# Kernel optimization log

Measured on AMD Instinct MI355X. Metric: run time of the kernel, lower is better.

The kernel has to match this reference:

```python
import jax, jax.numpy as jnp
import numpy as np

B, S, E, H = 4, 2048, 2048, 16
D = E // H  # head_dim = 128


def _rotary_tables():
    # standard interleaved RoPE: pairs (2i, 2i+1) share an angle
    inv_freq = 1.0 / (10000.0 ** (np.arange(0, D, 2, dtype=np.float64) / D))
    ang = np.arange(S, dtype=np.float64)[:, None] * inv_freq[None, :]  # [S, D/2]
    ang = np.repeat(ang, 2, axis=-1)  # [S, D]
    cos = np.cos(ang).astype(np.float32)[None, None]  # [1,1,S,D]
    sin = np.sin(ang).astype(np.float32)[None, None]
    return jnp.asarray(cos), jnp.asarray(sin)


def setup_inputs() -> dict:
    key = jax.random.key(0)
    ks = jax.random.split(key, 4)
    x = jax.random.normal(ks[0], (B, S, E), jnp.float32)
    cos, sin = _rotary_tables()
    Wqkv = jax.random.normal(ks[1], (E, 3 * E), jnp.float32) * 0.02
    bqkv = jnp.zeros((3 * E,), jnp.float32)
    Wproj = jax.random.normal(ks[2], (E, E), jnp.float32) * 0.02
    bproj = jnp.zeros((E,), jnp.float32)
    return {"x": x, "rotary_cos": cos, "rotary_sin": sin,
            "Wqkv": Wqkv, "bqkv": bqkv, "Wproj": Wproj, "bproj": bproj}


def apply_rotary(t, cos, sin):
    # t: [B,H,S,D]; interleaved rotate-half: (x1,x2) -> (-x2, x1)
    x1 = t[..., 0::2]
    x2 = t[..., 1::2]
    rot = jnp.stack((-x2, x1), axis=-1).reshape(t.shape)
    return t * cos + rot * sin


def reference(x, rotary_cos, rotary_sin, Wqkv, bqkv, Wproj, bproj):
    qkv = x @ Wqkv + bqkv  # [B,S,3E]
    q, k, v = jnp.split(qkv, 3, axis=-1)
    # [B,S,E] -> [B,H,S,D]
    to_heads = lambda t: t.reshape(B, S, H, D).transpose(0, 2, 1, 3)
    q, k, v = to_heads(q), to_heads(k), to_heads(v)
    q = apply_rotary(q, rotary_cos, rotary_sin)
    k = apply_rotary(k, rotary_cos, rotary_sin)
    scale = 1.0 / jnp.sqrt(jnp.float32(D))
    scores = jnp.einsum("bhqd,bhkd->bhqk", q, k) * scale  # non-causal
    attn = jax.nn.softmax(scores, axis=-1)
    y = jnp.einsum("bhqk,bhkd->bhqd", attn, v)
    y = y.transpose(0, 2, 1, 3).reshape(B, S, E)
    out = y @ Wproj + bproj
    return out, k, v
```

## Files before the change

### kernel.cpp

```cpp
#include <hip/hip_runtime.h>


typedef unsigned short u16;
typedef unsigned int   u32;
typedef float  f32x4  __attribute__((ext_vector_type(4)));
typedef __bf16 bf16x8 __attribute__((ext_vector_type(8)));

#define B_  4
#define S_  2048
#define E_  2048
#define H_  16
#define D_  128

__device__ __forceinline__ u16 f2bf(float f) {
    union { float f; u32 u; } v; v.f = f;
    return (u16)((v.u + 0x8000u) >> 16);
}
__device__ __forceinline__ u32 pack_bf(float a, float b) {
    union { float f; u32 u; } x, y; x.f = a; y.f = b;
    return ((x.u + 0x8000u) >> 16) | ((y.u + 0x8000u) & 0xFFFF0000u);
}
__device__ __forceinline__ float bf2f(u16 h) {
    union { u32 u; float f; } v; v.u = ((u32)h) << 16; return v.f;
}

__device__ __forceinline__ void gld16(const u16* g, u16* l) {
    __builtin_amdgcn_global_load_lds(
        (const __attribute__((address_space(1))) void*)g,
        (__attribute__((address_space(3))) void*)l, 16, 0, 0);
}

__global__ __launch_bounds__(256) void xconv_kernel(
    const float* __restrict__ x, u16* __restrict__ xb)
{
    size_t g = (size_t)blockIdx.x * 256 + threadIdx.x;
    const float4* p = (const float4*)x + g * 2;
    float4 a = p[0], b = p[1];
    uint4 pk;
    pk.x = pack_bf(a.x, a.y); pk.y = pack_bf(a.z, a.w);
    pk.z = pack_bf(b.x, b.y); pk.w = pack_bf(b.z, b.w);
    ((uint4*)xb)[g] = pk;
}

__global__ __launch_bounds__(256) void wtrans_kernel(
    const float* __restrict__ W, u16* __restrict__ WT, int K, int N)
{
    __shared__ float tile[64][65];
    const int n0 = blockIdx.x * 64, k0 = blockIdx.y * 64;
    const int t = threadIdx.x;
#pragma unroll
    for (int i = 0; i < 16; ++i) {
        int idx = i * 256 + t; int r = idx >> 6, c = idx & 63;
        tile[r][c] = W[(size_t)(k0 + r) * N + n0 + c];
    }
    __syncthreads();
#pragma unroll
    for (int i = 0; i < 16; ++i) {
        int idx = i * 256 + t; int rn = idx >> 6, ck = idx & 63;
        WT[(size_t)(n0 + rn) * K + k0 + ck] = f2bf(tile[ck][rn]);
    }
}

__device__ __forceinline__ void stage_half(
    const u16* __restrict__ g, int K, u16* l, int t)
{
    const int wb = (t >> 6) << 6;
#pragma unroll
    for (int j = 0; j < 2; ++j) {
        const int idx = j * 512 + t;
        const int row = idx >> 3, c = (idx & 7) ^ (row & 7);
        gld16(g + (size_t)row * K + (c << 3),
              l + ((j * 512 + wb) << 3));
    }
}

template <int MODE>
__global__ __launch_bounds__(512, 2) void gemm_kernel(
    const u16* __restrict__ A, const u16* __restrict__ Bt,
    const float* __restrict__ bias,
    u16* __restrict__ qh, u16* __restrict__ kh, u16* __restrict__ vt,
    float* __restrict__ vout, float* __restrict__ outf,
    int N, int K)
{
    __shared__ u16 Asm[2][256 * 64];
    __shared__ u16 Bsm[2][256 * 64];

    const int t = threadIdx.x;
    const int wave = t >> 6, lane = t & 63, quad = lane >> 4, l16 = lane & 15;
    const int wr = wave >> 2, wc = wave & 3;
    const int m0 = blockIdx.y * 256, n0 = blockIdx.x * 256;
    const int NT = K >> 6;

    const int sw0 = ((quad ^ (l16 & 7)) << 3);
    const int sw1 = (((4 + quad) ^ (l16 & 7)) << 3);
    const int aRow = (wr * 128 + l16) << 6;
    const int bRow = (wc * 64 + l16) << 6;

    f32x4 acc[8][4] = {};

    const u16* Ab = A  + (size_t)m0 * K;
    const u16* Bb = Bt + (size_t)n0 * K;

    stage_half(Ab,                        K, &Asm[0][0],    t);
    stage_half(Ab + (size_t)128 * K,      K, &Asm[0][8192], t);
    stage_half(Bb,                        K, &Bsm[0][0],    t);
    stage_half(Bb + (size_t)128 * K,      K, &Bsm[0][8192], t);
    stage_half(Ab + 64,                   K, &Asm[1][0],    t);
    stage_half(Ab + (size_t)128 * K + 64, K, &Asm[1][8192], t);
    asm volatile("s_waitcnt vmcnt(4)" ::: "memory");
    __builtin_amdgcn_s_barrier();

    for (int T = 0; T < NT; ++T) {
        const int cur = T & 1, nxt = cur ^ 1;
        const int kn1 = (T + 1) << 6, kn2 = (T + 2) << 6;
        const u16* Asb = &Asm[cur][0];
        const u16* Bsb = &Bsm[cur][0];
        bf16x8 af[8], b0, b1;

#pragma unroll
        for (int mi = 0; mi < 8; ++mi)
            af[mi] = *(const bf16x8*)(Asb + aRow + mi * 1024 + sw0);
        b0 = *(const bf16x8*)(Bsb + bRow + sw0);
        b1 = *(const bf16x8*)(Bsb + bRow + 1024 + sw0);
        if (T + 1 < NT) stage_half(Bb + kn1, K, &Bsm[nxt][0], t);
        __builtin_amdgcn_s_barrier();
        asm volatile("s_waitcnt lgkmcnt(0)" ::: "memory");
        __builtin_amdgcn_s_setprio(1);
#pragma unroll
        for (int mi = 0; mi < 8; ++mi) {
            acc[mi][0] = __builtin_amdgcn_mfma_f32_16x16x32_bf16(af[mi], b0, acc[mi][0], 0, 0, 0);
            acc[mi][1] = __builtin_amdgcn_mfma_f32_16x16x32_bf16(af[mi], b1, acc[mi][1], 0, 0, 0);
        }
        __builtin_amdgcn_s_setprio(0);
        __builtin_amdgcn_s_barrier();

        b0 = *(const bf16x8*)(Bsb + bRow + 2048 + sw0);
        b1 = *(const bf16x8*)(Bsb + bRow + 3072 + sw0);
        if (T + 1 < NT) stage_half(Bb + (size_t)128 * K + kn1, K, &Bsm[nxt][8192], t);
        __builtin_amdgcn_s_barrier();
        asm volatile("s_waitcnt lgkmcnt(0)" ::: "memory");
        __builtin_amdgcn_s_setprio(1);
#pragma unroll
        for (int mi = 0; mi < 8; ++mi) {
            acc[mi][2] = __builtin_amdgcn_mfma_f32_16x16x32_bf16(af[mi], b0, acc[mi][2], 0, 0, 0);
            acc[mi][3] = __builtin_amdgcn_mfma_f32_16x16x32_bf16(af[mi], b1, acc[mi][3], 0, 0, 0);
        }
        __builtin_amdgcn_s_setprio(0);
        __builtin_amdgcn_s_barrier();

#pragma unroll
        for (int mi = 0; mi < 8; ++mi)
            af[mi] = *(const bf16x8*)(Asb + aRow + mi * 1024 + sw1);
        b0 = *(const bf16x8*)(Bsb + bRow + sw1);
        b1 = *(const bf16x8*)(Bsb + bRow + 1024 + sw1);
        __builtin_amdgcn_s_barrier();
        asm volatile("s_waitcnt lgkmcnt(0)" ::: "memory");
        __builtin_amdgcn_s_setprio(1);
#pragma unroll
        for (int mi = 0; mi < 8; ++mi) {
            acc[mi][0] = __builtin_amdgcn_mfma_f32_16x16x32_bf16(af[mi], b0, acc[mi][0], 0, 0, 0);
            acc[mi][1] = __builtin_amdgcn_mfma_f32_16x16x32_bf16(af[mi], b1, acc[mi][1], 0, 0, 0);
        }
        __builtin_amdgcn_s_setprio(0);
        __builtin_amdgcn_s_barrier();

        b0 = *(const bf16x8*)(Bsb + bRow + 2048 + sw1);
        b1 = *(const bf16x8*)(Bsb + bRow + 3072 + sw1);
        if (T + 2 < NT) {
            stage_half(Ab + kn2,                   K, &Asm[cur][0],    t);
            stage_half(Ab + (size_t)128 * K + kn2, K, &Asm[cur][8192], t);
        }
        __builtin_amdgcn_s_barrier();
        asm volatile("s_waitcnt lgkmcnt(0)" ::: "memory");
        __builtin_amdgcn_s_setprio(1);
#pragma unroll
        for (int mi = 0; mi < 8; ++mi) {
            acc[mi][2] = __builtin_amdgcn_mfma_f32_16x16x32_bf16(af[mi], b0, acc[mi][2], 0, 0, 0);
            acc[mi][3] = __builtin_amdgcn_mfma_f32_16x16x32_bf16(af[mi], b1, acc[mi][3], 0, 0, 0);
        }
        __builtin_amdgcn_s_setprio(0);
        if (T + 2 < NT) { asm volatile("s_waitcnt vmcnt(4)" ::: "memory"); }
        else            { asm volatile("s_waitcnt vmcnt(0)" ::: "memory"); }
        __builtin_amdgcn_s_barrier();
    }

    if constexpr (MODE == 0) {
        const int sel = n0 >> 11;
        const int b   = m0 >> 11, sb = m0 & 2047;
#pragma unroll
        for (int ni = 0; ni < 4; ++ni) {
            const int dg = (n0 & 2047) + wc * 64 + ni * 16 + l16;
            const int h = dg >> 7, d = dg & 127;
            const float bv = bias[n0 + wc * 64 + ni * 16 + l16];
            const size_t hb = ((size_t)(b * H_ + h)) * S_ * D_;
#pragma unroll
            for (int mi = 0; mi < 8; ++mi) {
                const int s0 = sb + wr * 128 + mi * 16 + quad * 4;
                float v0 = acc[mi][ni][0] + bv, v1 = acc[mi][ni][1] + bv;
                float v2 = acc[mi][ni][2] + bv, v3 = acc[mi][ni][3] + bv;
                size_t base = hb + (size_t)s0 * D_ + d;
                if (sel < 2) {
                    u16* dst = sel ? kh : qh;
                    dst[base]        = f2bf(v0); dst[base + D_]    = f2bf(v1);
                    dst[base + 2*D_] = f2bf(v2); dst[base + 3*D_]  = f2bf(v3);
                } else {
                    vout[base] = v0; vout[base + D_] = v1;
                    vout[base + 2*D_] = v2; vout[base + 3*D_] = v3;
                    uint2 pk; pk.x = pack_bf(v0, v1); pk.y = pack_bf(v2, v3);
                    *(uint2*)(vt + ((size_t)(b * H_ + h) * D_ + d) * S_ + s0) = pk;
                }
            }
        }
    } else {
#pragma unroll
        for (int ni = 0; ni < 4; ++ni) {
            const int col = n0 + wc * 64 + ni * 16 + l16;
            const float bv = bias[col];
#pragma unroll
            for (int mi = 0; mi < 8; ++mi) {
                const int row0 = m0 + wr * 128 + mi * 16 + quad * 4;
#pragma unroll
                for (int r = 0; r < 4; ++r)
                    outf[(size_t)(row0 + r) * N + col] = acc[mi][ni][r] + bv;
            }
        }
    }
}

__global__ __launch_bounds__(256) void rotary_kernel(
    u16* __restrict__ q, u16* __restrict__ k, float* __restrict__ kout,
    const float* __restrict__ cosT, const float* __restrict__ sinT)
{
    const int g = blockIdx.x * 256 + threadIdx.x;
    const int d0 = (g & 15) << 3;
    const int srow = g >> 4;
    const int s = srow & (S_ - 1);
    const size_t base = (size_t)srow * D_ + d0;

    uint4 qv = *(const uint4*)(q + base);
    uint4 kv = *(const uint4*)(k + base);
    float cc[8], ss[8];
    *(float4*)(cc)     = *(const float4*)(cosT + s * D_ + d0);
    *(float4*)(cc + 4) = *(const float4*)(cosT + s * D_ + d0 + 4);
    *(float4*)(ss)     = *(const float4*)(sinT + s * D_ + d0);
    *(float4*)(ss + 4) = *(const float4*)(sinT + s * D_ + d0 + 4);
    const u16* qp = (const u16*)&qv; const u16* kp = (const u16*)&kv;
    float qo[8], ko[8];
#pragma unroll
    for (int i = 0; i < 4; ++i) {
        float q1 = bf2f(qp[2*i]), q2 = bf2f(qp[2*i+1]);
        float k1 = bf2f(kp[2*i]), k2 = bf2f(kp[2*i+1]);
        qo[2*i]   = q1 * cc[2*i]   - q2 * ss[2*i];
        qo[2*i+1] = q2 * cc[2*i+1] + q1 * ss[2*i+1];
        ko[2*i]   = k1 * cc[2*i]   - k2 * ss[2*i];
        ko[2*i+1] = k2 * cc[2*i+1] + k1 * ss[2*i+1];
    }
    const float qs_ = 0.08838834764831845f * 1.4426950408889634f;
    uint4 qpk, kpk;
    u32* qq = (u32*)&qpk; u32* kq = (u32*)&kpk;
#pragma unroll
    for (int i = 0; i < 4; ++i) {
        qq[i] = pack_bf(qo[2*i] * qs_, qo[2*i+1] * qs_);
        kq[i] = pack_bf(ko[2*i], ko[2*i+1]);
    }
    *(uint4*)(q + base) = qpk;
    *(uint4*)(k + base) = kpk;
    *(float4*)(kout + base)     = make_float4(ko[0], ko[1], ko[2], ko[3]);
    *(float4*)(kout + base + 4) = make_float4(ko[4], ko[5], ko[6], ko[7]);
}

#define KSWZ(row, c) ((row) * 128 + (((c) ^ ((row) & 7)) << 3))
#define VSWZ(d, c)   ((d) * 64 + (((c) ^ ((d) & 7)) << 3))
#define PSWZ(qr, c)  ((qr) * 64 + (((c) ^ ((qr) & 7)) << 3))

__global__ __launch_bounds__(256, 4) void attn_kernel(
    const u16* __restrict__ qh, const u16* __restrict__ kh,
    const u16* __restrict__ vt, u16* __restrict__ yb)
{
    __shared__ u16 Ks[64 * 128];
    __shared__ u16 Vs[128 * 64];
    __shared__ u16 Ps[4 * 16 * 64];

    const int t = threadIdx.x, wave = t >> 6, lane = t & 63;
    const int quad = lane >> 4, l16 = lane & 15;
    const int bh = blockIdx.y, q0 = blockIdx.x * 64;
    const u16* kb = kh + (size_t)bh * S_ * D_;
    const u16* vb = vt + (size_t)bh * D_ * S_;
    u16* Pw = Ps + wave * (16 * 64);

    bf16x8 qf[4];
    {
        const u16* qp = qh + ((size_t)bh * S_ + q0 + wave * 16 + l16) * D_ + quad * 8;
#pragma unroll
        for (int kk = 0; kk < 4; ++kk) qf[kk] = *(const bf16x8*)(qp + kk * 32);
    }

    f32x4 o[8] = {};
    float m_r = -1e30f, l_r = 0.f;

    for (int k0 = 0; k0 < S_; k0 += 64) {
        __syncthreads();
#pragma unroll
        for (int i = 0; i < 4; ++i) {
            int idx = i * 256 + t;
            {
                int row = idx >> 4, c = (idx & 15) ^ (row & 7);
                gld16(kb + (size_t)(k0 + row) * D_ + (c << 3),
                      Ks + ((i * 256 + wave * 64) << 3));
            }
            {
                int d = idx >> 3, c = (idx & 7) ^ (d & 7);
                gld16(vb + (size_t)d * S_ + k0 + (c << 3),
                      Vs + ((i * 256 + wave * 64) << 3));
            }
        }
        __syncthreads();

        f32x4 sc[4] = {};
#pragma unroll
        for (int kk = 0; kk < 4; ++kk) {
#pragma unroll
            for (int nt = 0; nt < 4; ++nt) {
                bf16x8 kf = *(const bf16x8*)(Ks + KSWZ(nt * 16 + l16, kk * 4 + quad));
                sc[nt] = __builtin_amdgcn_mfma_f32_16x16x32_bf16(kf, qf[kk], sc[nt], 0, 0, 0);
            }
        }
        float mx = sc[0][0];
#pragma unroll
        for (int nt = 0; nt < 4; ++nt)
#pragma unroll
            for (int r = 0; r < 4; ++r) mx = fmaxf(mx, sc[nt][r]);
        mx = fmaxf(mx, __shfl_xor(mx, 16));
        mx = fmaxf(mx, __shfl_xor(mx, 32));
        float mn = fmaxf(m_r, mx);
        float alpha = exp2f(m_r - mn);
        m_r = mn;
        float rs = 0.f;
#pragma unroll
        for (int nt = 0; nt < 4; ++nt)
#pragma unroll
            for (int r = 0; r < 4; ++r) {
                float p = exp2f(sc[nt][r] - mn);
                sc[nt][r] = p; rs += p;
            }
        rs += __shfl_xor(rs, 16);
        rs += __shfl_xor(rs, 32);
        l_r = l_r * alpha + rs;
        float af4[4];
#pragma unroll
        for (int r = 0; r < 4; ++r) af4[r] = __shfl(alpha, quad * 4 + r);
#pragma unroll
        for (int dt = 0; dt < 8; ++dt)
#pragma unroll
            for (int r = 0; r < 4; ++r) o[dt][r] *= af4[r];

#pragma unroll
        for (int nt = 0; nt < 4; ++nt) {
            int key0 = nt * 16 + quad * 4;
            int chunk = key0 >> 3, sub = key0 & 7;
            uint2 pk;
            pk.x = pack_bf(sc[nt][0], sc[nt][1]);
            pk.y = pack_bf(sc[nt][2], sc[nt][3]);
            *(uint2*)(Pw + PSWZ(l16, chunk) + sub) = pk;
        }
#pragma unroll
        for (int kk2 = 0; kk2 < 2; ++kk2) {
            bf16x8 pf = *(const bf16x8*)(Pw + PSWZ(l16, kk2 * 4 + quad));
#pragma unroll
            for (int dt = 0; dt < 8; ++dt) {
                bf16x8 vf = *(const bf16x8*)(Vs + VSWZ(dt * 16 + l16, kk2 * 4 + quad));
                o[dt] = __builtin_amdgcn_mfma_f32_16x16x32_bf16(pf, vf, o[dt], 0, 0, 0);
            }
        }
    }
    float lf[4];
#pragma unroll
    for (int r = 0; r < 4; ++r) {
        float lv = __shfl(l_r, quad * 4 + r);
        lf[r] = __builtin_amdgcn_rcpf(lv);
    }
    const int b = bh >> 4, h = bh & 15;
#pragma unroll
    for (int dt = 0; dt < 8; ++dt) {
        int d = h * D_ + dt * 16 + l16;
#pragma unroll
        for (int r = 0; r < 4; ++r) {
            int s = q0 + wave * 16 + quad * 4 + r;
            yb[(size_t)(b * S_ + s) * E_ + d] = f2bf(o[dt][r] * lf[r]);
        }
    }
}

extern "C" void kernel_launch(void* const* d_in, const int* in_sizes, int n_in,
                              void* d_out, int out_size, void* d_ws, size_t ws_size,
                              hipStream_t stream)
{
    (void)in_sizes; (void)n_in; (void)out_size; (void)ws_size;
    const float* x     = (const float*)d_in[0];
    const float* cosT  = (const float*)d_in[1];
    const float* sinT  = (const float*)d_in[2];
    const float* Wqkv  = (const float*)d_in[3];
    const float* bqkv  = (const float*)d_in[4];
    const float* Wproj = (const float*)d_in[5];
    const float* bproj = (const float*)d_in[6];

    float* out  = (float*)d_out;
    float* kout = out  + (size_t)B_ * S_ * E_;
    float* vout = kout + (size_t)B_ * S_ * E_;

    u16* wqkvT  = (u16*)d_ws;
    u16* wprojT = wqkvT  + (size_t)12582912;
    u16* qh     = wprojT + (size_t)4194304;
    u16* kh     = qh     + (size_t)16777216;
    u16* vt     = kh     + (size_t)16777216;
    u16* yb     = vt     + (size_t)16777216;
    u16* xb     = yb;

    xconv_kernel<<<8192, 256, 0, stream>>>(x, xb);
    wtrans_kernel<<<dim3(96, 32), 256, 0, stream>>>(Wqkv, wqkvT, 2048, 6144);
    wtrans_kernel<<<dim3(32, 32), 256, 0, stream>>>(Wproj, wprojT, 2048, 2048);
    gemm_kernel<0><<<dim3(24, 32), 512, 0, stream>>>(
        xb, wqkvT, bqkv, qh, kh, vt, vout, nullptr, 6144, 2048);
    rotary_kernel<<<8192, 256, 0, stream>>>(qh, kh, kout, cosT, sinT);
    attn_kernel<<<dim3(32, 64), 256, 0, stream>>>(qh, kh, vt, yb);
    gemm_kernel<1><<<dim3(8, 32), 512, 0, stream>>>(
        yb, wprojT, bproj, nullptr, nullptr, nullptr, nullptr, out, 2048, 2048);
}
```

Baseline: 843.9 us.

## Double-buffer K/V tiles in attention, add lazy rescale and MFMA priority

Splits the K/V shared-memory tiles into two buffers so the next tile's global-to-LDS loads are issued before computing on the current tile, with one wait and barrier per iteration instead of two syncthreads. It also skips the online-softmax rescale of the accumulator when the running max grows by at most 8 (in log2 units) across the wave, and raises wave priority around the MFMA blocks. The larger LDS footprint lowers the occupancy hint from 4 to 2 blocks per CU. The lazy rescale lets unnormalised exponentials reach up to 2^8 in bf16 P, which could cost some accuracy.

```diff
diff --git a/kernel.cpp b/kernel.cpp
--- a/kernel.cpp
+++ b/kernel.cpp
@@ -273,12 +273,12 @@
 #define VSWZ(d, c)   ((d) * 64 + (((c) ^ ((d) & 7)) << 3))
 #define PSWZ(qr, c)  ((qr) * 64 + (((c) ^ ((qr) & 7)) << 3))
 
-__global__ __launch_bounds__(256, 4) void attn_kernel(
+__global__ __launch_bounds__(256, 2) void attn_kernel(
     const u16* __restrict__ qh, const u16* __restrict__ kh,
     const u16* __restrict__ vt, u16* __restrict__ yb)
 {
-    __shared__ u16 Ks[64 * 128];
-    __shared__ u16 Vs[128 * 64];
+    __shared__ u16 Ks[2][64 * 128];
+    __shared__ u16 Vs[2][64 * 128];
     __shared__ u16 Ps[4 * 16 * 64];
 
     const int t = threadIdx.x, wave = t >> 6, lane = t & 63;
@@ -288,43 +288,53 @@
     const u16* vb = vt + (size_t)bh * D_ * S_;
     u16* Pw = Ps + wave * (16 * 64);
 
-    bf16x8 qf[4];
-    {
-        const u16* qp = qh + ((size_t)bh * S_ + q0 + wave * 16 + l16) * D_ + quad * 8;
-#pragma unroll
-        for (int kk = 0; kk < 4; ++kk) qf[kk] = *(const bf16x8*)(qp + kk * 32);
-    }
-
-    f32x4 o[8] = {};
-    float m_r = -1e30f, l_r = 0.f;
-
-    for (int k0 = 0; k0 < S_; k0 += 64) {
-        __syncthreads();
+    auto stage = [&](int buf, int k0) {
 #pragma unroll
         for (int i = 0; i < 4; ++i) {
             int idx = i * 256 + t;
             {
                 int row = idx >> 4, c = (idx & 15) ^ (row & 7);
                 gld16(kb + (size_t)(k0 + row) * D_ + (c << 3),
-                      Ks + ((i * 256 + wave * 64) << 3));
+                      &Ks[buf][0] + ((i * 256 + wave * 64) << 3));
             }
             {
                 int d = idx >> 3, c = (idx & 7) ^ (d & 7);
                 gld16(vb + (size_t)d * S_ + k0 + (c << 3),
-                      Vs + ((i * 256 + wave * 64) << 3));
-            }
-        }
-        __syncthreads();
+                      &Vs[buf][0] + ((i * 256 + wave * 64) << 3));
+            }
+        }
+    };
+
+    bf16x8 qf[4];
+    {
+        const u16* qp = qh + ((size_t)bh * S_ + q0 + wave * 16 + l16) * D_ + quad * 8;
+#pragma unroll
+        for (int kk = 0; kk < 4; ++kk) qf[kk] = *(const bf16x8*)(qp + kk * 32);
+    }
+
+    f32x4 o[8] = {};
+    float m_r = -1e30f, l_r = 0.f;
+
+    stage(0, 0);
+    asm volatile("s_waitcnt vmcnt(0)" ::: "memory");
+    __builtin_amdgcn_s_barrier();
+
+    for (int k0 = 0; k0 < S_; k0 += 64) {
+        const int cur = (k0 >> 6) & 1;
+        if (k0 + 64 < S_) stage(cur ^ 1, k0 + 64);
 
         f32x4 sc[4] = {};
+        __builtin_amdgcn_s_setprio(1);
 #pragma unroll
         for (int kk = 0; kk < 4; ++kk) {
 #pragma unroll
             for (int nt = 0; nt < 4; ++nt) {
-                bf16x8 kf = *(const bf16x8*)(Ks + KSWZ(nt * 16 + l16, kk * 4 + quad));
+                bf16x8 kf = *(const bf16x8*)(&Ks[cur][0] + KSWZ(nt * 16 + l16, kk * 4 + quad));
                 sc[nt] = __builtin_amdgcn_mfma_f32_16x16x32_bf16(kf, qf[kk], sc[nt], 0, 0, 0);
             }
         }
+        __builtin_amdgcn_s_setprio(0);
+
         float mx = sc[0][0];
 #pragma unroll
         for (int nt = 0; nt < 4; ++nt)
@@ -332,27 +342,30 @@
             for (int r = 0; r < 4; ++r) mx = fmaxf(mx, sc[nt][r]);
         mx = fmaxf(mx, __shfl_xor(mx, 16));
         mx = fmaxf(mx, __shfl_xor(mx, 32));
-        float mn = fmaxf(m_r, mx);
-        float alpha = exp2f(m_r - mn);
-        m_r = mn;
+        if (!__all(mx - m_r <= 8.0f)) {
+            float mn = fmaxf(m_r, mx);
+            float alpha = exp2f(m_r - mn);
+            m_r = mn;
+            l_r *= alpha;
+            float af4[4];
+#pragma unroll
+            for (int r = 0; r < 4; ++r) af4[r] = __shfl(alpha, quad * 4 + r);
+#pragma unroll
+            for (int dt = 0; dt < 8; ++dt)
+#pragma unroll
+                for (int r = 0; r < 4; ++r) o[dt][r] *= af4[r];
+        }
         float rs = 0.f;
 #pragma unroll
         for (int nt = 0; nt < 4; ++nt)
 #pragma unroll
             for (int r = 0; r < 4; ++r) {
-                float p = exp2f(sc[nt][r] - mn);
+                float p = exp2f(sc[nt][r] - m_r);
                 sc[nt][r] = p; rs += p;
             }
         rs += __shfl_xor(rs, 16);
         rs += __shfl_xor(rs, 32);
-        l_r = l_r * alpha + rs;
-        float af4[4];
-#pragma unroll
-        for (int r = 0; r < 4; ++r) af4[r] = __shfl(alpha, quad * 4 + r);
-#pragma unroll
-        for (int dt = 0; dt < 8; ++dt)
-#pragma unroll
-            for (int r = 0; r < 4; ++r) o[dt][r] *= af4[r];
+        l_r += rs;
 
 #pragma unroll
         for (int nt = 0; nt < 4; ++nt) {
@@ -363,15 +376,20 @@
             pk.y = pack_bf(sc[nt][2], sc[nt][3]);
             *(uint2*)(Pw + PSWZ(l16, chunk) + sub) = pk;
         }
+        __builtin_amdgcn_s_setprio(1);
 #pragma unroll
         for (int kk2 = 0; kk2 < 2; ++kk2) {
             bf16x8 pf = *(const bf16x8*)(Pw + PSWZ(l16, kk2 * 4 + quad));
 #pragma unroll
             for (int dt = 0; dt < 8; ++dt) {
-                bf16x8 vf = *(const bf16x8*)(Vs + VSWZ(dt * 16 + l16, kk2 * 4 + quad));
+                bf16x8 vf = *(const bf16x8*)(&Vs[cur][0] + VSWZ(dt * 16 + l16, kk2 * 4 + quad));
                 o[dt] = __builtin_amdgcn_mfma_f32_16x16x32_bf16(pf, vf, o[dt], 0, 0, 0);
             }
         }
+        __builtin_amdgcn_s_setprio(0);
+
+        asm volatile("s_waitcnt vmcnt(0)" ::: "memory");
+        __builtin_amdgcn_s_barrier();
     }
     float lf[4];
 #pragma unroll
```

Measured after the change: 895.5 us. +6.1%, slower.

## Prefetch next K/V tile into registers and add lazy softmax rescaling

Applied to the files above, without the earlier changes.

Replaces the direct global-to-LDS loads with register prefetch of the next K/V tile, issued before the current tile's compute and written to LDS after it. This is meant to hide global load latency behind the MFMA work. It also skips the output rescale when the running max grows by no more than a threshold, uses tree reductions for the max and sum, and raises wave priority around the MFMA blocks. In exchange, the prefetch adds 32 VGPRs per thread, which may reduce occupancy at launch bounds of 4. The lazy rescale lets exp2 values exceed 1 by up to 2^8, so bf16 P values can grow.

```diff
diff --git a/kernel.cpp b/kernel.cpp
--- a/kernel.cpp
+++ b/kernel.cpp
@@ -288,6 +288,25 @@
     const u16* vb = vt + (size_t)bh * D_ * S_;
     u16* Pw = Ps + wave * (16 * 64);
 
+    const int krow = t >> 4, kc = t & 15;
+    const int vrow = t >> 3, vc = t & 7;
+    uint4 gk[4], gv[4];
+
+    auto stage_load = [&](int k0) {
+#pragma unroll
+        for (int i = 0; i < 4; ++i) {
+            gk[i] = *(const uint4*)(kb + (size_t)(k0 + i * 16 + krow) * D_ + (kc << 3));
+            gv[i] = *(const uint4*)(vb + (size_t)(i * 32 + vrow) * S_ + k0 + (vc << 3));
+        }
+    };
+    auto stage_write = [&]() {
+#pragma unroll
+        for (int i = 0; i < 4; ++i) {
+            *(uint4*)(Ks + KSWZ(i * 16 + krow, kc)) = gk[i];
+            *(uint4*)(Vs + VSWZ(i * 32 + vrow, vc)) = gv[i];
+        }
+    };
+
     bf16x8 qf[4];
     {
         const u16* qp = qh + ((size_t)bh * S_ + q0 + wave * 16 + l16) * D_ + quad * 8;
@@ -298,25 +317,16 @@
     f32x4 o[8] = {};
     float m_r = -1e30f, l_r = 0.f;
 
+    stage_load(0);
+    stage_write();
+    __syncthreads();
+
     for (int k0 = 0; k0 < S_; k0 += 64) {
-        __syncthreads();
-#pragma unroll
-        for (int i = 0; i < 4; ++i) {
-            int idx = i * 256 + t;
-            {
-                int row = idx >> 4, c = (idx & 15) ^ (row & 7);
-                gld16(kb + (size_t)(k0 + row) * D_ + (c << 3),
-                      Ks + ((i * 256 + wave * 64) << 3));
-            }
-            {
-                int d = idx >> 3, c = (idx & 7) ^ (d & 7);
-                gld16(vb + (size_t)d * S_ + k0 + (c << 3),
-                      Vs + ((i * 256 + wave * 64) << 3));
-            }
-        }
-        __syncthreads();
+        const bool more = (k0 + 64 < S_);
+        if (more) stage_load(k0 + 64);
 
         f32x4 sc[4] = {};
+        __builtin_amdgcn_s_setprio(1);
 #pragma unroll
         for (int kk = 0; kk < 4; ++kk) {
 #pragma unroll
@@ -325,34 +335,40 @@
                 sc[nt] = __builtin_amdgcn_mfma_f32_16x16x32_bf16(kf, qf[kk], sc[nt], 0, 0, 0);
             }
         }
-        float mx = sc[0][0];
-#pragma unroll
-        for (int nt = 0; nt < 4; ++nt)
-#pragma unroll
-            for (int r = 0; r < 4; ++r) mx = fmaxf(mx, sc[nt][r]);
+        __builtin_amdgcn_s_setprio(0);
+
+        float m0a = fmaxf(fmaxf(sc[0][0], sc[0][1]), fmaxf(sc[0][2], sc[0][3]));
+        float m1a = fmaxf(fmaxf(sc[1][0], sc[1][1]), fmaxf(sc[1][2], sc[1][3]));
+        float m2a = fmaxf(fmaxf(sc[2][0], sc[2][1]), fmaxf(sc[2][2], sc[2][3]));
+        float m3a = fmaxf(fmaxf(sc[3][0], sc[3][1]), fmaxf(sc[3][2], sc[3][3]));
+        float mx = fmaxf(fmaxf(m0a, m1a), fmaxf(m2a, m3a));
         mx = fmaxf(mx, __shfl_xor(mx, 16));
         mx = fmaxf(mx, __shfl_xor(mx, 32));
-        float mn = fmaxf(m_r, mx);
-        float alpha = exp2f(m_r - mn);
-        m_r = mn;
-        float rs = 0.f;
-#pragma unroll
-        for (int nt = 0; nt < 4; ++nt)
-#pragma unroll
-            for (int r = 0; r < 4; ++r) {
-                float p = exp2f(sc[nt][r] - mn);
-                sc[nt][r] = p; rs += p;
-            }
+        if (!__all(mx - m_r <= 8.0f)) {
+            float mn = fmaxf(m_r, mx);
+            float alpha = exp2f(m_r - mn);
+            m_r = mn;
+            l_r *= alpha;
+            float af4[4];
+#pragma unroll
+            for (int r = 0; r < 4; ++r) af4[r] = __shfl(alpha, quad * 4 + r);
+#pragma unroll
+            for (int dt = 0; dt < 8; ++dt)
+#pragma unroll
+                for (int r = 0; r < 4; ++r) o[dt][r] *= af4[r];
+        }
+        float rsp[4];
+#pragma unroll
+        for (int nt = 0; nt < 4; ++nt) {
+#pragma unroll
+            for (int r = 0; r < 4; ++r)
+                sc[nt][r] = exp2f(sc[nt][r] - m_r);
+            rsp[nt] = (sc[nt][0] + sc[nt][1]) + (sc[nt][2] + sc[nt][3]);
+        }
+        float rs = (rsp[0] + rsp[1]) + (rsp[2] + rsp[3]);
         rs += __shfl_xor(rs, 16);
         rs += __shfl_xor(rs, 32);
-        l_r = l_r * alpha + rs;
-        float af4[4];
-#pragma unroll
-        for (int r = 0; r < 4; ++r) af4[r] = __shfl(alpha, quad * 4 + r);
-#pragma unroll
-        for (int dt = 0; dt < 8; ++dt)
-#pragma unroll
-            for (int r = 0; r < 4; ++r) o[dt][r] *= af4[r];
+        l_r += rs;
 
 #pragma unroll
         for (int nt = 0; nt < 4; ++nt) {
@@ -363,6 +379,7 @@
             pk.y = pack_bf(sc[nt][2], sc[nt][3]);
             *(uint2*)(Pw + PSWZ(l16, chunk) + sub) = pk;
         }
+        __builtin_amdgcn_s_setprio(1);
 #pragma unroll
         for (int kk2 = 0; kk2 < 2; ++kk2) {
             bf16x8 pf = *(const bf16x8*)(Pw + PSWZ(l16, kk2 * 4 + quad));
@@ -371,6 +388,13 @@
                 bf16x8 vf = *(const bf16x8*)(Vs + VSWZ(dt * 16 + l16, kk2 * 4 + quad));
                 o[dt] = __builtin_amdgcn_mfma_f32_16x16x32_bf16(pf, vf, o[dt], 0, 0, 0);
             }
+        }
+        __builtin_amdgcn_s_setprio(0);
+
+        __syncthreads();
+        if (more) {
+            stage_write();
+            __syncthreads();
         }
     }
     float lf[4];
```

New measurement: 1.332 ms. 57.8% more time.
